# Optimization experiments

Measured on AMD Instinct MI355X. Metric: run time of the kernel, lower is better.

## Reference

```python
import jax, jax.numpy as jnp
from jax import lax
import numpy as np

INPUT_SIZE = 256
HIDDEN = 256


def _gru_scan(x, W_ih, W_hh, b_ih, b_hh):
    # x: [b, t, in], PyTorch GRU gate order: r, z, n
    b, t, _ = x.shape
    k = W_hh.shape[1]
    # precompute input contribution for all timesteps: [b, t, 3k]
    gx = jnp.einsum('bti,gi->btg', x, W_ih) + b_ih

    def step(h, gxt):
        gh = h @ W_hh.T + b_hh                 # [b, 3k]
        xr, xz, xn = jnp.split(gxt, 3, axis=-1)
        hr, hz, hn = jnp.split(gh, 3, axis=-1)
        r = jax.nn.sigmoid(xr + hr)
        z = jax.nn.sigmoid(xz + hz)
        n = jnp.tanh(xn + r * hn)
        h_new = (1.0 - z) * n + z * h
        return h_new, h_new

    h0 = jnp.zeros((b, k), x.dtype)
    _, hs = lax.scan(step, h0, jnp.swapaxes(gx, 0, 1))  # hs: [t, b, k]
    return hs


def setup_inputs() -> dict:
    key = jax.random.key(0)
    kx, k1, k2, k3, k4 = jax.random.split(key, 5)
    s_ih = 1.0 / np.sqrt(HIDDEN)
    x = jax.random.normal(kx, (32, 2048, INPUT_SIZE), dtype=jnp.float32)
    W_ih = jax.random.uniform(k1, (3 * HIDDEN, INPUT_SIZE), jnp.float32, -s_ih, s_ih)
    W_hh = jax.random.uniform(k2, (3 * HIDDEN, HIDDEN), jnp.float32, -s_ih, s_ih)
    b_ih = jax.random.uniform(k3, (3 * HIDDEN,), jnp.float32, -s_ih, s_ih)
    b_hh = jax.random.uniform(k4, (3 * HIDDEN,), jnp.float32, -s_ih, s_ih)
    return {'x': x, 'W_ih': W_ih, 'W_hh': W_hh, 'b_ih': b_ih, 'b_hh': b_hh}


def reference(x, W_ih, W_hh, b_ih, b_hh):
    # forward direction
    hs_f = _gru_scan(x, W_ih, W_hh, b_ih, b_hh)                     # [t, b, k]
    # 'bidirectional': same weights applied to time-reversed input
    hs_r = _gru_scan(x[:, ::-1, :], W_ih, W_hh, b_ih, b_hh)[::-1]   # [t, b, k]
    outputs = jnp.concatenate(
        (jnp.swapaxes(hs_f, 0, 1), jnp.swapaxes(hs_r, 0, 1)), axis=2)  # [b, t, 2k]
    hiddens = jnp.concatenate((hs_f, hs_r), axis=2)                    # [t, b, 2k]
    return outputs, hiddens
```

## Files before the change

kernel.cpp:

```cpp
#include <hip/hip_runtime.h>
#include <hip/hip_fp16.h>


typedef __fp16 half2_t __attribute__((ext_vector_type(2)));

static constexpr int T_STEPS = 2048;
static constexpr int BATCH   = 32;
static constexpr int HID     = 256;
static constexpr int IN      = 256;
static constexpr int G3      = 768;

__device__ __forceinline__ float fdot2(half2_t a, half2_t b, float c) {
    return __builtin_amdgcn_fdot2(a, b, c, false);
}

__device__ __forceinline__ void barrier_lgkm() {
    asm volatile("s_waitcnt lgkmcnt(0)\n\ts_barrier" ::: "memory");
}

__global__ __launch_bounds__(256, 2) void gx_gemm(
        const float* __restrict__ x,
        const float* __restrict__ Wih,
        const float* __restrict__ bih,
        const float* __restrict__ bhh,
        _Float16* __restrict__ gx) {
    __shared__ ushort As[64 * 256];
    __shared__ ushort Bs[64 * 256];

    const int tid = threadIdx.x;
    const int m0  = blockIdx.x * 64;
    const int tx  = tid & 15;
    const int ty  = tid >> 4;

#pragma unroll
    for (int i = 0; i < 16; ++i) {
        int f    = tid + 256 * i;
        int row  = f >> 6;
        int col4 = f & 63;
        float4 v = *(const float4*)(x + (size_t)(m0 + row) * IN + col4 * 4);
        half2_t h0 = __builtin_amdgcn_cvt_pkrtz(v.x, v.y);
        half2_t h1 = __builtin_amdgcn_cvt_pkrtz(v.z, v.w);
        int chunk = col4 >> 1;
        int idx = row * 256 + ((chunk ^ (row & 7)) * 8) + (col4 & 1) * 4;
        uint2 wv;
        wv.x = __builtin_bit_cast(unsigned, h0);
        wv.y = __builtin_bit_cast(unsigned, h1);
        *(uint2*)(As + idx) = wv;
    }

    for (int nb = 0; nb < 12; ++nb) {
#pragma unroll
        for (int i = 0; i < 16; ++i) {
            int f    = tid + 256 * i;
            int row  = f >> 6;
            int col4 = f & 63;
            float4 v = *(const float4*)(Wih + (size_t)(nb * 64 + row) * IN + col4 * 4);
            half2_t h0 = __builtin_amdgcn_cvt_pkrtz(v.x, v.y);
            half2_t h1 = __builtin_amdgcn_cvt_pkrtz(v.z, v.w);
            int chunk = col4 >> 1;
            int idx = row * 256 + ((chunk ^ (row & 7)) * 8) + (col4 & 1) * 4;
            uint2 wv;
            wv.x = __builtin_bit_cast(unsigned, h0);
            wv.y = __builtin_bit_cast(unsigned, h1);
            *(uint2*)(Bs + idx) = wv;
        }
        barrier_lgkm();

        float acc[4][4];
#pragma unroll
        for (int jm = 0; jm < 4; ++jm)
#pragma unroll
            for (int jn = 0; jn < 4; ++jn) acc[jm][jn] = 0.f;

#pragma unroll 4
        for (int kc = 0; kc < 32; ++kc) {
            union { uint4 u; half2_t h[4]; } av[4], bv[4];
#pragma unroll
            for (int jm = 0; jm < 4; ++jm) {
                int r = ty * 4 + jm;
                av[jm].u = *(const uint4*)(As + r * 256 + ((kc ^ (r & 7)) * 8));
            }
#pragma unroll
            for (int jn = 0; jn < 4; ++jn) {
                int r = tx + 16 * jn;
                bv[jn].u = *(const uint4*)(Bs + r * 256 + ((kc ^ (r & 7)) * 8));
            }
#pragma unroll
            for (int jm = 0; jm < 4; ++jm)
#pragma unroll
                for (int jn = 0; jn < 4; ++jn)
#pragma unroll
                    for (int p = 0; p < 4; ++p)
                        acc[jm][jn] = fdot2(av[jm].h[p], bv[jn].h[p], acc[jm][jn]);
        }

#pragma unroll
        for (int jn = 0; jn < 4; ++jn) {
            int n = nb * 64 + tx + 16 * jn;
            float bias = bih[n] + (n < 512 ? bhh[n] : 0.f);
#pragma unroll
            for (int jm = 0; jm < 4; ++jm) {
                int m = m0 + ty * 4 + jm;
                gx[(size_t)m * G3 + n] = (_Float16)(acc[jm][jn] + bias);
            }
        }
        barrier_lgkm();
    }
}

__attribute__((amdgpu_waves_per_eu(1, 3)))
__global__ __launch_bounds__(768) void gru_seq(
        const _Float16* __restrict__ gx,
        const float* __restrict__ Whh,
        const float* __restrict__ bhh,
        float* __restrict__ out0,
        float* __restrict__ out1) {
    __shared__ float  P[4 * 768];
    __shared__ ushort h16[256];
    __shared__ ushort gxb[768];

    const int tid = threadIdx.x;
    const int b   = blockIdx.x & 31;
    const int d   = blockIdx.x >> 5;
    const int w   = tid >> 6;
    const int L   = tid & 63;
    const int s   = w & 3;
    const int g   = w >> 2;

    half2_t Wr[4][32];
    float   Wb[4];
#pragma unroll
    for (int jr = 0; jr < 4; ++jr) {
        const int row = g * 256 + jr * 64 + L;
        const float* wrow = Whh + (size_t)row * HID + s * 64;
#pragma unroll
        for (int q = 0; q < 32; ++q) {
            float2 wv = *(const float2*)(wrow + 2 * q);
            Wr[jr][q] = __builtin_amdgcn_cvt_pkrtz(wv.x, wv.y);
        }
        Wb[jr] = (s == 0 && row >= 512) ? bhh[row] : 0.f;
    }

    float hprev = 0.f;
    if (tid < 256) h16[tid] = 0;

    const int tp0 = d ? (T_STEPS - 1) : 0;
    const int sgn = d ? -1 : 1;

    const _Float16* gp = gx + ((size_t)b * T_STEPS + tp0) * G3 + tid * 8;
    const int gpd = sgn * G3;
    uint4 greg{};
    if (tid < 96) greg = *(const uint4*)gp;

    float* o0 = out0 + ((size_t)b * T_STEPS + tp0) * 512 + d * 256 + tid;
    float* o1 = out1 + ((size_t)tp0 * BATCH + b) * 512 + d * 256 + tid;
    const int o0d = sgn * 512;
    const int o1d = sgn * (BATCH * 512);

    __syncthreads();

    for (int t = 0; t < T_STEPS; ++t) {
        if (tid < 96) {
            *(uint4*)(gxb + tid * 8) = greg;
            if (t + 1 < T_STEPS) {
                gp += gpd;
                greg = *(const uint4*)gp;
            }
        }

        float acc[4] = {Wb[0], Wb[1], Wb[2], Wb[3]};
#pragma unroll
        for (int c = 0; c < 4; ++c) {
            union { uint4 u; half2_t h[4]; } hh0, hh1;
            hh0.u = *(const uint4*)(h16 + s * 64 + c * 16);
            hh1.u = *(const uint4*)(h16 + s * 64 + c * 16 + 8);
#pragma unroll
            for (int jr = 0; jr < 4; ++jr) {
#pragma unroll
                for (int p = 0; p < 4; ++p) {
                    acc[jr] = fdot2(Wr[jr][c * 8 + p],     hh0.h[p], acc[jr]);
                    acc[jr] = fdot2(Wr[jr][c * 8 + 4 + p], hh1.h[p], acc[jr]);
                }
            }
        }
#pragma unroll
        for (int jr = 0; jr < 4; ++jr)
            P[s * 768 + g * 256 + jr * 64 + L] = acc[jr];

        barrier_lgkm();

        if (tid < 256) {
            const int i = tid;
            float hr = (P[i]       + P[768 + i])  + (P[1536 + i] + P[2304 + i]);
            float hz = (P[256 + i] + P[1024 + i]) + (P[1792 + i] + P[2560 + i]);
            float hn = (P[512 + i] + P[1280 + i]) + (P[2048 + i] + P[2816 + i]);
            const _Float16* gxh = (const _Float16*)gxb;
            float xr = (float)gxh[i]       + hr;
            float xz = (float)gxh[256 + i] + hz;
            float r = __builtin_amdgcn_rcpf(1.f + __builtin_amdgcn_exp2f(xr * -1.44269504f));
            float z = __builtin_amdgcn_rcpf(1.f + __builtin_amdgcn_exp2f(xz * -1.44269504f));
            float nx = (float)gxh[512 + i] + r * hn;
            float e2 = __builtin_amdgcn_exp2f(nx * 2.88539008f);
            float n  = 1.f - 2.f * __builtin_amdgcn_rcpf(1.f + e2);
            float h  = n + z * (hprev - n);
            hprev = h;

            h16[i] = __builtin_bit_cast(ushort, (_Float16)h);
            *o0 = h; *o1 = h;
            o0 += o0d; o1 += o1d;
        }
        barrier_lgkm();
    }
}

extern "C" void kernel_launch(void* const* d_in, const int* in_sizes, int n_in,
                              void* d_out, int out_size, void* d_ws, size_t ws_size,
                              hipStream_t stream) {
    const float* x   = (const float*)d_in[0];
    const float* Wih = (const float*)d_in[1];
    const float* Whh = (const float*)d_in[2];
    const float* bih = (const float*)d_in[3];
    const float* bhh = (const float*)d_in[4];

    float* out0 = (float*)d_out;
    float* out1 = out0 + (size_t)BATCH * T_STEPS * 512;

    _Float16* gx = (_Float16*)d_ws;

    gx_gemm<<<dim3(65536 / 64), dim3(256), 0, stream>>>(x, Wih, bih, bhh, gx);
    gru_seq<<<dim3(BATCH * 2), dim3(768), 0, stream>>>(gx, Whh, bhh, out0, out1);
}
```

Before: 2.558 ms.

## Assign one full W_hh row per thread in GRU recurrence to drop partial-sum reduction

Each of the 768 threads now holds a complete W_hh row (128 packed half2 registers) instead of four quarter-rows, so the per-step hidden matvec needs no cross-wave partial-sum reduction through shared memory. The combine step reads a single gh value per gate instead of summing four partials. The gx prefetch moves to threads 512-607, which sit outside the 256 gate-update threads, so loads overlap with the gate math. The h vector reads now broadcast the same addresses to all lanes. The cost is the same register footprint with a longer per-thread dependency chain and heavier shared-memory broadcast reads.

```diff
diff --git a/kernel.cpp b/kernel.cpp
--- a/kernel.cpp
+++ b/kernel.cpp
@@ -115,31 +115,25 @@
         const float* __restrict__ bhh,
         float* __restrict__ out0,
         float* __restrict__ out1) {
-    __shared__ float  P[4 * 768];
+    __shared__ float  gh[768];
     __shared__ ushort h16[256];
     __shared__ ushort gxb[768];
 
     const int tid = threadIdx.x;
     const int b   = blockIdx.x & 31;
     const int d   = blockIdx.x >> 5;
-    const int w   = tid >> 6;
-    const int L   = tid & 63;
-    const int s   = w & 3;
-    const int g   = w >> 2;
-
-    half2_t Wr[4][32];
-    float   Wb[4];
-#pragma unroll
-    for (int jr = 0; jr < 4; ++jr) {
-        const int row = g * 256 + jr * 64 + L;
-        const float* wrow = Whh + (size_t)row * HID + s * 64;
-#pragma unroll
-        for (int q = 0; q < 32; ++q) {
+    const int row = tid;
+
+    half2_t Wr[128];
+    {
+        const float* wrow = Whh + (size_t)row * HID;
+#pragma unroll
+        for (int q = 0; q < 128; ++q) {
             float2 wv = *(const float2*)(wrow + 2 * q);
-            Wr[jr][q] = __builtin_amdgcn_cvt_pkrtz(wv.x, wv.y);
-        }
-        Wb[jr] = (s == 0 && row >= 512) ? bhh[row] : 0.f;
-    }
+            Wr[q] = __builtin_amdgcn_cvt_pkrtz(wv.x, wv.y);
+        }
+    }
+    const float Wb = (row >= 512) ? bhh[row] : 0.f;
 
     float hprev = 0.f;
     if (tid < 256) h16[tid] = 0;
@@ -147,53 +141,51 @@
     const int tp0 = d ? (T_STEPS - 1) : 0;
     const int sgn = d ? -1 : 1;
 
-    const _Float16* gp = gx + ((size_t)b * T_STEPS + tp0) * G3 + tid * 8;
+    const int pt = tid - 512;
+    const bool pf = (unsigned)pt < 96u;
+    const _Float16* gp = gx + ((size_t)b * T_STEPS + tp0) * G3 + (pf ? pt * 8 : 0);
     const int gpd = sgn * G3;
     uint4 greg{};
-    if (tid < 96) greg = *(const uint4*)gp;
-
-    float* o0 = out0 + ((size_t)b * T_STEPS + tp0) * 512 + d * 256 + tid;
-    float* o1 = out1 + ((size_t)tp0 * BATCH + b) * 512 + d * 256 + tid;
+    if (pf) greg = *(const uint4*)gp;
+
+    float* o0 = out0 + ((size_t)b * T_STEPS + tp0) * 512 + d * 256 + (tid & 255);
+    float* o1 = out1 + ((size_t)tp0 * BATCH + b) * 512 + d * 256 + (tid & 255);
     const int o0d = sgn * 512;
     const int o1d = sgn * (BATCH * 512);
 
     __syncthreads();
 
     for (int t = 0; t < T_STEPS; ++t) {
-        if (tid < 96) {
-            *(uint4*)(gxb + tid * 8) = greg;
+        if (pf) {
+            *(uint4*)(gxb + pt * 8) = greg;
             if (t + 1 < T_STEPS) {
                 gp += gpd;
                 greg = *(const uint4*)gp;
             }
         }
 
-        float acc[4] = {Wb[0], Wb[1], Wb[2], Wb[3]};
+        float acc[4] = {Wb, 0.f, 0.f, 0.f};
 #pragma unroll
         for (int c = 0; c < 4; ++c) {
-            union { uint4 u; half2_t h[4]; } hh0, hh1;
-            hh0.u = *(const uint4*)(h16 + s * 64 + c * 16);
-            hh1.u = *(const uint4*)(h16 + s * 64 + c * 16 + 8);
-#pragma unroll
-            for (int jr = 0; jr < 4; ++jr) {
-#pragma unroll
-                for (int p = 0; p < 4; ++p) {
-                    acc[jr] = fdot2(Wr[jr][c * 8 + p],     hh0.h[p], acc[jr]);
-                    acc[jr] = fdot2(Wr[jr][c * 8 + 4 + p], hh1.h[p], acc[jr]);
-                }
-            }
-        }
-#pragma unroll
-        for (int jr = 0; jr < 4; ++jr)
-            P[s * 768 + g * 256 + jr * 64 + L] = acc[jr];
+            union { uint4 u; half2_t h[4]; } hv[8];
+#pragma unroll
+            for (int j = 0; j < 8; ++j)
+                hv[j].u = *(const uint4*)(h16 + c * 64 + j * 8);
+#pragma unroll
+            for (int j = 0; j < 8; ++j)
+#pragma unroll
+                for (int p = 0; p < 4; ++p)
+                    acc[c] = fdot2(Wr[c * 32 + j * 4 + p], hv[j].h[p], acc[c]);
+        }
+        gh[row] = (acc[0] + acc[1]) + (acc[2] + acc[3]);
 
         barrier_lgkm();
 
         if (tid < 256) {
             const int i = tid;
-            float hr = (P[i]       + P[768 + i])  + (P[1536 + i] + P[2304 + i]);
-            float hz = (P[256 + i] + P[1024 + i]) + (P[1792 + i] + P[2560 + i]);
-            float hn = (P[512 + i] + P[1280 + i]) + (P[2048 + i] + P[2816 + i]);
+            float hr = gh[i];
+            float hz = gh[256 + i];
+            float hn = gh[512 + i];
             const _Float16* gxh = (const _Float16*)gxb;
             float xr = (float)gxh[i]       + hr;
             float xz = (float)gxh[256 + i] + hz;
```

Measured after the change: 2.804 ms. 1.1x slower.
